# Kernel optimization log

Measured on AMD Instinct MI355X. Metric: run time of the kernel, lower is better.

Reference implementation:

```python
import jax, jax.numpy as jnp
import numpy as np

COMMITMENT_COST = 0.25

def _conv(x, w, stride, pad):
    return jax.lax.conv_general_dilated(
        x, w, window_strides=(stride, stride),
        padding=((pad, pad), (pad, pad)),
        dimension_numbers=("NCHW", "OIHW", "NCHW"))

def _gelu(x):
    return jax.nn.gelu(x, approximate=False)

def setup_inputs() -> dict:
    key = jax.random.key(0)
    ks = jax.random.split(key, 9)
    def w(k, shape):
        fan_in = shape[1] * shape[2] * shape[3]
        return jax.random.normal(k, shape, jnp.float32) / jnp.sqrt(fan_in)
    return {
        "x": jax.random.normal(ks[0], (32, 3, 256, 256), jnp.float32),
        "enc_w1": w(ks[1], (64, 3, 5, 5)),
        "enc_w2": w(ks[2], (64, 64, 5, 5)),
        "enc_w3": w(ks[3], (64, 64, 2, 2)),
        "dec_w1": w(ks[4], (512, 64, 2, 2)),
        "dec_w2": w(ks[5], (256, 512, 2, 2)),
        "dec_w3": w(ks[6], (256, 256, 2, 2)),
        "codes": jax.random.normal(ks[7], (24, 64), jnp.float32),
        "ema_count": jax.random.uniform(ks[8], (24,), jnp.float32) + 0.1,
    }

def reference(x, enc_w1, enc_w2, enc_w3, dec_w1, dec_w2, dec_w3, codes, ema_count):
    # ---- encoder: 256 -> 128 -> 64 -> 63, channels 3 -> 64 ----
    z = _conv(x, enc_w1, 2, 2)
    z = _gelu(z)
    z = _conv(z, enc_w2, 2, 2)
    z = _gelu(z)
    z = _conv(z, enc_w3, 1, 0)          # [B, 64, 63, 63]

    # ---- VQ codebook (EMA variant: commitment loss only) ----
    B, C, H, W = z.shape
    zf = jnp.transpose(z, (0, 2, 3, 1)).reshape(-1, C)          # [N, C]
    # squared L2 distances to each code
    d = (jnp.sum(zf * zf, axis=1, keepdims=True)
         - 2.0 * zf @ codes.T
         + jnp.sum(codes * codes, axis=1))                       # [N, K]
    idx = jnp.argmin(d, axis=1)                                  # [N]
    zq = codes[idx].reshape(B, H, W, C).transpose(0, 3, 1, 2)    # [B, C, H, W]

    vq_loss = COMMITMENT_COST * jnp.mean(
        (jax.lax.stop_gradient(zq) - z) ** 2)
    # straight-through estimator
    z_hat = z + jax.lax.stop_gradient(zq - z)

    # code probabilities from EMA cluster counts, gathered per position
    probs = ema_count / jnp.sum(ema_count)                       # [K]
    z_probs = probs[idx].reshape(B, H, W)                        # [B, H, W]

    # ---- decoder: 63 -> 64 -> 63 -> 64, channels 64 -> 512 -> 256 -> 256 ----
    y = _conv(z_hat, dec_w1, 1, 1)
    y = _gelu(y)
    y = _conv(y, dec_w2, 1, 0)
    y = _gelu(y)
    x_hat = _conv(y, dec_w3, 1, 1)      # [B, 256, 64, 64]

    return (x_hat, z_probs, vq_loss)
```

## Files before the change

### kernel.cpp

```cpp
#include <hip/hip_runtime.h>
#include <hip/hip_bf16.h>


#define DEV_INLINE __device__ __forceinline__

typedef __attribute__((ext_vector_type(8))) short bf16x8;
typedef __attribute__((ext_vector_type(4))) float f32x4;

#define GLL16(g, l) __builtin_amdgcn_global_load_lds(                      \
    (const __attribute__((address_space(1))) void*)(g),                    \
    (__attribute__((address_space(3))) void*)(l), 16, 0, 0)

DEV_INLINE float gelu_exact(float v) {
    return 0.5f * v * (1.0f + erff(v * 0.70710678118654752440f));
}

__global__ void wtf_k(const float* __restrict__ w, float* __restrict__ wt,
                      int C, int total) {
    int t = blockIdx.x * 256 + threadIdx.x;
    if (t >= total) return;
    int oc = t & 63;
    int rest = t >> 6;
    int tap = rest % 25, c = rest / 25;
    wt[t] = w[(oc * C + c) * 25 + tap];
}

template<int C, int IH, int IW>
__global__ __launch_bounds__(256) void conv5s2_t(
    const float* __restrict__ xg,
    const float* __restrict__ wt,
    float* __restrict__ outg) {
    constexpr int OH = IH / 2, OW = IW / 2;
    __shared__ float xin[35 * 36];
    __shared__ float wl[1600];
    const int tid = threadIdx.x;
    const int n = blockIdx.z;
    const int OY0 = blockIdx.y * 16, OX0 = blockIdx.x * 16;
    const int IY0 = OY0 * 2 - 2, IX0 = OX0 * 2 - 2;
    const int og = tid & 3;
    const int pg = tid >> 2;
    const int py = (pg >> 3) * 2, px = (pg & 7) * 2;
    const int ry = py * 2, rx = px * 2;

    f32x4 a00 = {0,0,0,0}, a01 = a00, a02 = a00, a03 = a00;
    f32x4 a10 = a00, a11 = a00, a12 = a00, a13 = a00;
    f32x4 a20 = a00, a21 = a00, a22 = a00, a23 = a00;
    f32x4 a30 = a00, a31 = a00, a32 = a00, a33 = a00;

    const float* xn = xg + (size_t)n * C * IH * IW;
    for (int c = 0; c < C; ++c) {
        {
            const float4* wsrc = (const float4*)(wt + c * 1600);
            float4* wdst = (float4*)wl;
            wdst[tid] = wsrc[tid];
            if (tid < 144) wdst[256 + tid] = wsrc[256 + tid];
        }
        const float* zc = xn + (size_t)c * IH * IW;
        for (int i = tid; i < 1225; i += 256) {
            int r = i / 35, cl = i - r * 35;
            int iy = IY0 + r, ix = IX0 + cl;
            float v = 0.f;
            if ((unsigned)iy < (unsigned)IH && (unsigned)ix < (unsigned)IW)
                v = zc[(size_t)iy * IW + ix];
            xin[r * 36 + cl] = v;
        }
        __syncthreads();
#pragma unroll
        for (int ky = 0; ky < 5; ++ky) {
            const float* r0 = xin + (ry + ky) * 36 + rx;
            const float* r1 = r0 + 72;
#pragma unroll
            for (int kx = 0; kx < 5; ++kx) {
                const f32x4* wq = (const f32x4*)(wl + (ky * 5 + kx) * 64 + og * 16);
                f32x4 w0 = wq[0], w1 = wq[1], w2 = wq[2], w3 = wq[3];
                float xA = r0[kx], xB = r0[kx + 2];
                float xC = r1[kx], xD = r1[kx + 2];
                a00 += xA * w0; a01 += xA * w1; a02 += xA * w2; a03 += xA * w3;
                a10 += xB * w0; a11 += xB * w1; a12 += xB * w2; a13 += xB * w3;
                a20 += xC * w0; a21 += xC * w1; a22 += xC * w2; a23 += xC * w3;
                a30 += xD * w0; a31 += xD * w1; a32 += xD * w2; a33 += xD * w3;
            }
        }
        __syncthreads();
    }
    const int ocb = og * 16;
#define CSTORE(v, oy, ox, q) {                                                \
        float* o = outg + (((size_t)n * 64 + ocb + (q) * 4) * OH + (oy)) * OW \
                   + (ox);                                                    \
        o[0]               = gelu_exact((v).x);                               \
        o[(size_t)OH * OW]     = gelu_exact((v).y);                           \
        o[(size_t)2 * OH * OW] = gelu_exact((v).z);                           \
        o[(size_t)3 * OH * OW] = gelu_exact((v).w); }
    CSTORE(a00, OY0 + py,     OX0 + px,     0); CSTORE(a01, OY0 + py,     OX0 + px,     1);
    CSTORE(a02, OY0 + py,     OX0 + px,     2); CSTORE(a03, OY0 + py,     OX0 + px,     3);
    CSTORE(a10, OY0 + py,     OX0 + px + 1, 0); CSTORE(a11, OY0 + py,     OX0 + px + 1, 1);
    CSTORE(a12, OY0 + py,     OX0 + px + 1, 2); CSTORE(a13, OY0 + py,     OX0 + px + 1, 3);
    CSTORE(a20, OY0 + py + 1, OX0 + px,     0); CSTORE(a21, OY0 + py + 1, OX0 + px,     1);
    CSTORE(a22, OY0 + py + 1, OX0 + px,     2); CSTORE(a23, OY0 + py + 1, OX0 + px,     3);
    CSTORE(a30, OY0 + py + 1, OX0 + px + 1, 0); CSTORE(a31, OY0 + py + 1, OX0 + px + 1, 1);
    CSTORE(a32, OY0 + py + 1, OX0 + px + 1, 2); CSTORE(a33, OY0 + py + 1, OX0 + px + 1, 3);
#undef CSTORE
}

template<int C, int IH, int IW>
__global__ __launch_bounds__(256, 4) void conv5s2_g(
    const float* __restrict__ xg,
    const float* __restrict__ wt,
    float* __restrict__ outg) {
    constexpr int OH = IH / 2, OW = IW / 2;
    __shared__ float xp[760];
    const int tid = threadIdx.x;
    const int n = blockIdx.z;
    const int OY0 = blockIdx.y * 8, OX0 = blockIdx.x * 16;
    const int IY0 = OY0 * 2 - 2, IX0 = OX0 * 2 - 2;
    const int og = tid & 15;
    const int pg = tid >> 4;
    const int py = (pg >> 2) * 2;
    const int px = (pg & 3) * 4;
    const int ry = py * 2;

    int  sG[3]; int sL[3]; bool sIn[3]; bool sWr[3];
#pragma unroll
    for (int k = 0; k < 3; ++k) {
        int s = tid + k * 256;
        int r = s / 36, cl = s - r * 36;
        int iy = IY0 + r, ix = IX0 + cl;
        sWr[k] = (s < 684);
        sIn[k] = sWr[k] && ((unsigned)iy < (unsigned)IH) &&
                 ((unsigned)ix < (unsigned)IW);
        sG[k] = sIn[k] ? (iy * IW + ix) : 0;
        sL[k] = sWr[k] ? ((cl & 1) * 380 + r * 20 + (cl >> 1)) : 0;
    }

    const float* xn = xg + (size_t)n * C * IH * IW;
    const float* wtb = wt + og * 4;

    f32x4 a00 = {0,0,0,0}, a01 = a00, a02 = a00, a03 = a00;
    f32x4 a10 = a00, a11 = a00, a12 = a00, a13 = a00;

    for (int c = 0; c < C; ++c) {
        const float* zc = xn + (size_t)c * IH * IW;
#pragma unroll
        for (int k = 0; k < 3; ++k) {
            if (sWr[k]) {
                float v = sIn[k] ? zc[sG[k]] : 0.f;
                xp[sL[k]] = v;
            }
        }
        __syncthreads();

        const float* wc = wtb + (size_t)c * 1600;
#define PICK8(Qa, Qb, i) ((i) < 4 ? (Qa)[(i) & 3] : (Qb)[(i) & 3])
#define XV(R, kx, jj) (((kx) & 1)                                           \
        ? PICK8(O##R##0, O##R##1, (jj) + ((kx) >> 1))                       \
        : PICK8(E##R##0, E##R##1, (jj) + ((kx) >> 1)))
#pragma unroll
        for (int ky = 0; ky < 5; ++ky) {
            f32x4 w0 = *(const f32x4*)(wc + (ky * 5 + 0) * 64);
            f32x4 w1 = *(const f32x4*)(wc + (ky * 5 + 1) * 64);
            f32x4 w2 = *(const f32x4*)(wc + (ky * 5 + 2) * 64);
            f32x4 w3 = *(const f32x4*)(wc + (ky * 5 + 3) * 64);
            f32x4 w4 = *(const f32x4*)(wc + (ky * 5 + 4) * 64);
            const float* e0 = xp + (ry + ky) * 20 + px;
            const float* o0 = e0 + 380;
            const float* e1 = e0 + 40;
            const float* o1 = o0 + 40;
            const f32x4 E00 = *(const f32x4*)e0, E01 = *(const f32x4*)(e0 + 4);
            const f32x4 O00 = *(const f32x4*)o0, O01 = *(const f32x4*)(o0 + 4);
            const f32x4 E10 = *(const f32x4*)e1, E11 = *(const f32x4*)(e1 + 4);
            const f32x4 O10 = *(const f32x4*)o1, O11 = *(const f32x4*)(o1 + 4);
#pragma unroll
            for (int kx = 0; kx < 5; ++kx) {
                const f32x4 wv = (kx == 0) ? w0 : (kx == 1) ? w1
                               : (kx == 2) ? w2 : (kx == 3) ? w3 : w4;
                float xA = XV(0, kx, 0), xB = XV(0, kx, 1);
                float xC = XV(0, kx, 2), xD = XV(0, kx, 3);
                float xE = XV(1, kx, 0), xF = XV(1, kx, 1);
                float xG = XV(1, kx, 2), xH = XV(1, kx, 3);
                a00 += xA * wv; a01 += xB * wv; a02 += xC * wv; a03 += xD * wv;
                a10 += xE * wv; a11 += xF * wv; a12 += xG * wv; a13 += xH * wv;
            }
        }
#undef XV
#undef PICK8
        __syncthreads();
    }

    const size_t HW = (size_t)OH * OW;
#pragma unroll
    for (int j = 0; j < 4; ++j) {
        float* o = outg + ((size_t)n * 64 + og * 4 + j) * HW
                   + (size_t)(OY0 + py) * OW + (OX0 + px);
        f32x4 t0, t1;
        t0[0] = gelu_exact(a00[j]); t0[1] = gelu_exact(a01[j]);
        t0[2] = gelu_exact(a02[j]); t0[3] = gelu_exact(a03[j]);
        t1[0] = gelu_exact(a10[j]); t1[1] = gelu_exact(a11[j]);
        t1[2] = gelu_exact(a12[j]); t1[3] = gelu_exact(a13[j]);
        *(f32x4*)o = t0;
        *(f32x4*)(o + OW) = t1;
    }
}

__global__ void conv3_k(const float* __restrict__ z2,
                        const float* __restrict__ w,
                        float* __restrict__ z) {
    __shared__ float wl[1024];
    const int oc0 = blockIdx.y * 4;
    for (int i = threadIdx.x; i < 1024; i += 256) {
        int j = i & 3, r = i >> 2;
        wl[i] = w[(oc0 + j) * 256 + r];
    }
    __syncthreads();
    const int s = blockIdx.x * 256 + threadIdx.x;
    if (s >= 3969) return;
    const int n = blockIdx.z;
    const int oy = s / 63, ox = s % 63;
    const float4* wv = (const float4*)wl;
    float a0 = 0.f, a1 = 0.f, a2 = 0.f, a3 = 0.f;
    const float* zn = z2 + n * 64 * 4096;
    for (int c = 0; c < 64; ++c) {
        const float* zc = zn + c * 4096;
#pragma unroll
        for (int tap = 0; tap < 4; ++tap) {
            int iy = oy + (tap >> 1), ix = ox + (tap & 1);
            float xv = zc[iy * 64 + ix];
            float4 wq = wv[c * 4 + tap];
            a0 += xv * wq.x; a1 += xv * wq.y; a2 += xv * wq.z; a3 += xv * wq.w;
        }
    }
    int obase = (n * 64 + oc0) * 3969 + s;
    z[obase]            = a0;
    z[obase + 3969]     = a1;
    z[obase + 2 * 3969] = a2;
    z[obase + 3 * 3969] = a3;
}

__global__ void vq_k(const float* __restrict__ z,
                     const float* __restrict__ codes,
                     const float* __restrict__ ema,
                     int* __restrict__ idxO,
                     float* __restrict__ zprobsO,
                     float* __restrict__ lossO) {
    __shared__ float cl[1536];
    __shared__ float cn[24];
    __shared__ float pr[24];
    for (int i = threadIdx.x; i < 1536; i += 256) cl[i] = codes[i];
    if (threadIdx.x < 24) pr[threadIdx.x] = ema[threadIdx.x];
    __syncthreads();
    if (threadIdx.x < 24) {
        float sm = 0.f;
        for (int c = 0; c < 64; ++c) { float v = cl[threadIdx.x * 64 + c]; sm += v * v; }
        cn[threadIdx.x] = sm;
    }
    __syncthreads();
    int t = blockIdx.x * 256 + threadIdx.x;
    float l = 0.f;
    if (t < 127008) {
        int b = t / 3969, s = t - b * 3969;
        const float* zp = z + (b * 64) * 3969 + s;
        float zv[64];
        float zn = 0.f;
#pragma unroll
        for (int c = 0; c < 64; ++c) { float v = zp[c * 3969]; zv[c] = v; zn += v * v; }
        float best = 1e30f; int bi = 0;
        for (int k = 0; k < 24; ++k) {
            float dot = 0.f;
#pragma unroll
            for (int c = 0; c < 64; ++c) dot += zv[c] * cl[k * 64 + c];
            float d = zn - 2.f * dot + cn[k];
            if (d < best) { best = d; bi = k; }
        }
        idxO[t] = bi;
        float psum = 0.f;
        for (int k = 0; k < 24; ++k) psum += pr[k];
        zprobsO[t] = pr[bi] / psum;
        for (int c = 0; c < 64; ++c) { float dd = cl[bi * 64 + c] - zv[c]; l += dd * dd; }
    }
    for (int off = 32; off; off >>= 1) l += __shfl_down(l, off, 64);
    if ((threadIdx.x & 63) == 0) atomicAdd(lossO, l);
}

__global__ void dtab_k(const float* __restrict__ codes,
                       const float* __restrict__ w1,
                       float* __restrict__ D) {
    int t = blockIdx.x * 256 + threadIdx.x;
    if (t >= 24 * 4 * 512) return;
    int oc = t & 511, tap = (t >> 9) & 3, k = t >> 11;
    float acc = 0.f;
    for (int c = 0; c < 64; ++c)
        acc += codes[k * 64 + c] * w1[oc * 256 + c * 4 + tap];
    D[t] = acc;
}

__global__ void wt_k(const float* __restrict__ w, __hip_bfloat16* __restrict__ wT,
                     int cl2, int total) {
    int t = blockIdx.x * 256 + threadIdx.x;
    if (t >= total) return;
    int c = t & ((1 << cl2) - 1);
    int tap = (t >> cl2) & 3;
    int oc = t >> (cl2 + 2);
    wT[t] = __float2bfloat16(w[((oc << cl2) + c) * 4 + tap]);
}

__global__ void dec1_k(const int* __restrict__ idx,
                       const float* __restrict__ D,
                       __hip_bfloat16* __restrict__ y1) {
    const int pos = blockIdx.x;
    const int n = pos >> 12, rem = pos & 4095;
    const int iy = rem >> 6, ix = rem & 63;
    const int* idn = idx + n * 3969;
    const int t = threadIdx.x;
    float ax = 0.f, ay = 0.f;
#pragma unroll
    for (int tap = 0; tap < 4; ++tap) {
        int py = iy - 1 + (tap >> 1), px = ix - 1 + (tap & 1);
        if ((unsigned)py < 63u && (unsigned)px < 63u) {
            int k = idn[py * 63 + px];
            float2 v = ((const float2*)(D + (k * 4 + tap) * 512))[t];
            ax += v.x; ay += v.y;
        }
    }
    __hip_bfloat162 o;
    o.x = __float2bfloat16(gelu_exact(ax));
    o.y = __float2bfloat16(gelu_exact(ay));
    ((__hip_bfloat162*)(y1 + (size_t)pos * 512))[t] = o;
}

__global__ __launch_bounds__(256) void dec2_mfma(
    const __hip_bfloat16* __restrict__ y1,
    const __hip_bfloat16* __restrict__ wT,
    const __hip_bfloat16* __restrict__ zp,
    __hip_bfloat16* __restrict__ y2)
{
    __shared__ __hip_bfloat16 As[128 * 32];
    __shared__ __hip_bfloat16 Bs[128 * 32];
    const int tid = threadIdx.x;
    const int wave = tid >> 6, lane = tid & 63;
    const int quad = lane >> 4, l15 = lane & 15;
    const int m0 = blockIdx.x * 128;
    const int oc0 = blockIdx.y * 128;
    const int sub = tid & 3;

    const char* pA[2];
    const char* pB[2];
#pragma unroll
    for (int j = 0; j < 2; ++j) {
        int slot = j * 64 + (tid >> 2);
        int pp = m0 + slot;
        if (pp < 127008) {
            int n = pp / 3969; int r = pp - n * 3969;
            int oy = r / 63;  int ox = r - oy * 63;
            pA[j] = (const char*)y1 + (size_t)((n * 64 + oy) * 64 + ox) * 1024 + sub * 16;
        } else {
            pA[j] = (const char*)zp;
        }
        pB[j] = (const char*)wT + (size_t)(oc0 + slot) * 4096 + sub * 16;
    }
    char* ldsA[2] = {(char*)As + wave * 1024, (char*)As + 4096 + wave * 1024};
    char* ldsB[2] = {(char*)Bs + wave * 1024, (char*)Bs + 4096 + wave * 1024};

    f32x4 acc[4][4] = {};
    const int wm = (wave & 1) * 64;
    const int wn = (wave >> 1) * 64;

#pragma unroll
    for (int tap = 0; tap < 4; ++tap) {
        const int toff = ((tap >> 1) * 64 + (tap & 1)) * 1024;
        for (int kk = 0; kk < 16; ++kk) {
            const int cb = kk * 64;
            GLL16(pA[0] + toff + cb, ldsA[0]);
            GLL16(pA[1] + toff + cb, ldsA[1]);
            GLL16(pB[0] + tap * 1024 + cb, ldsB[0]);
            GLL16(pB[1] + tap * 1024 + cb, ldsB[1]);
            __syncthreads();
            bf16x8 af[4], bf[4];
#pragma unroll
            for (int mi = 0; mi < 4; ++mi)
                af[mi] = *(const bf16x8*)((const char*)As + (wm + mi * 16 + l15) * 64 + quad * 16);
#pragma unroll
            for (int ni = 0; ni < 4; ++ni)
                bf[ni] = *(const bf16x8*)((const char*)Bs + (wn + ni * 16 + l15) * 64 + quad * 16);
#pragma unroll
            for (int mi = 0; mi < 4; ++mi)
#pragma unroll
                for (int ni = 0; ni < 4; ++ni)
                    acc[mi][ni] = __builtin_amdgcn_mfma_f32_16x16x32_bf16(
                        af[mi], bf[ni], acc[mi][ni], 0, 0, 0);
            __syncthreads();
        }
    }
#pragma unroll
    for (int mi = 0; mi < 4; ++mi)
#pragma unroll
        for (int r = 0; r < 4; ++r) {
            int pos = m0 + wm + mi * 16 + quad * 4 + r;
            if (pos < 127008) {
#pragma unroll
                for (int ni = 0; ni < 4; ++ni) {
                    int oc = oc0 + wn + ni * 16 + l15;
                    y2[(size_t)pos * 256 + oc] =
                        __float2bfloat16(gelu_exact(acc[mi][ni][r]));
                }
            }
        }
}

__global__ __launch_bounds__(256) void dec3_mfma(
    const __hip_bfloat16* __restrict__ y2,
    const __hip_bfloat16* __restrict__ wT,
    const __hip_bfloat16* __restrict__ zp,
    float* __restrict__ out)
{
    __shared__ __hip_bfloat16 As[128 * 32];
    __shared__ __hip_bfloat16 Bs[128 * 32];
    const int tid = threadIdx.x;
    const int wave = tid >> 6, lane = tid & 63;
    const int quad = lane >> 4, l15 = lane & 15;
    const int p0 = blockIdx.x * 128;
    const int oc0 = blockIdx.y * 128;
    const int sub = tid & 3;

    const char* pW[2];
    const char* pP[4][2];
#pragma unroll
    for (int j = 0; j < 2; ++j) {
        int slot = j * 64 + (tid >> 2);
        pW[j] = (const char*)wT + (size_t)(oc0 + slot) * 2048 + sub * 16;
        int pp = p0 + slot;
        int n = pp >> 12, rem = pp & 4095;
        int OY = rem >> 6, OX = rem & 63;
#pragma unroll
        for (int tap = 0; tap < 4; ++tap) {
            int iy = OY - 1 + (tap >> 1), ix = OX - 1 + (tap & 1);
            if ((unsigned)iy < 63u && (unsigned)ix < 63u)
                pP[tap][j] = (const char*)y2 + (size_t)(n * 3969 + iy * 63 + ix) * 512 + sub * 16;
            else
                pP[tap][j] = (const char*)zp;
        }
    }
    char* ldsA[2] = {(char*)As + wave * 1024, (char*)As + 4096 + wave * 1024};
    char* ldsB[2] = {(char*)Bs + wave * 1024, (char*)Bs + 4096 + wave * 1024};

    f32x4 acc[4][4] = {};
    const int wm = (wave & 1) * 64;
    const int wn = (wave >> 1) * 64;

#pragma unroll
    for (int tap = 0; tap < 4; ++tap) {
        for (int kk = 0; kk < 8; ++kk) {
            const int cb = kk * 64;
            GLL16(pW[0] + tap * 512 + cb, ldsA[0]);
            GLL16(pW[1] + tap * 512 + cb, ldsA[1]);
            GLL16(pP[tap][0] + cb, ldsB[0]);
            GLL16(pP[tap][1] + cb, ldsB[1]);
            __syncthreads();
            bf16x8 af[4], bf[4];
#pragma unroll
            for (int mi = 0; mi < 4; ++mi)
                af[mi] = *(const bf16x8*)((const char*)As + (wm + mi * 16 + l15) * 64 + quad * 16);
#pragma unroll
            for (int ni = 0; ni < 4; ++ni)
                bf[ni] = *(const bf16x8*)((const char*)Bs + (wn + ni * 16 + l15) * 64 + quad * 16);
#pragma unroll
            for (int mi = 0; mi < 4; ++mi)
#pragma unroll
                for (int ni = 0; ni < 4; ++ni)
                    acc[mi][ni] = __builtin_amdgcn_mfma_f32_16x16x32_bf16(
                        af[mi], bf[ni], acc[mi][ni], 0, 0, 0);
            __syncthreads();
        }
    }
    const int n = p0 >> 12;
    const int posLocal0 = (p0 & 4095) + wn;
#pragma unroll
    for (int mi = 0; mi < 4; ++mi)
#pragma unroll
        for (int r = 0; r < 4; ++r) {
            int oc = oc0 + wm + mi * 16 + quad * 4 + r;
            float* orow = out + ((size_t)(n * 256 + oc) << 12);
#pragma unroll
            for (int ni = 0; ni < 4; ++ni)
                orow[posLocal0 + ni * 16 + l15] = acc[mi][ni][r];
        }
}

__global__ void loss_k(const float* __restrict__ lossO, float* __restrict__ out) {
    out[0] = 0.25f * lossO[0] / 8128512.0f;
}

extern "C" void kernel_launch(void* const* d_in, const int* in_sizes, int n_in,
                              void* d_out, int out_size, void* d_ws, size_t ws_size,
                              hipStream_t stream) {
    const float* x     = (const float*)d_in[0];
    const float* ew1   = (const float*)d_in[1];
    const float* ew2   = (const float*)d_in[2];
    const float* ew3   = (const float*)d_in[3];
    const float* dw1   = (const float*)d_in[4];
    const float* dw2   = (const float*)d_in[5];
    const float* dw3   = (const float*)d_in[6];
    const float* codes = (const float*)d_in[7];
    const float* ema   = (const float*)d_in[8];
    float* out = (float*)d_out;

    char* ws = (char*)d_ws;
    float* z1   = (float*)(ws + 0);
    float* z2   = (float*)(ws + 134217728);
    float* z    = (float*)(ws + 167772160);
    int*   idx  = (int*)  (ws + 200286208);
    float* loss = (float*)(ws + 200794240);
    __hip_bfloat16* zp  = (__hip_bfloat16*)(ws + 200794496);
    float* D    = (float*)(ws + 200864128);
    __hip_bfloat16* wT2 = (__hip_bfloat16*)(ws + 201650560);
    __hip_bfloat16* wT3 = (__hip_bfloat16*)(ws + 202699136);
    float* wt2f = (float*)(ws + 201650560);
    float* wt1f = (float*)(ws + 202699136);
    __hip_bfloat16* y1  = (__hip_bfloat16*)(ws + 0);
    __hip_bfloat16* y2  = (__hip_bfloat16*)(ws + 134217728);

    hipMemsetAsync(loss, 0, 4, stream);
    hipMemsetAsync(zp, 0, 69632, stream);

    wtf_k<<<dim3(19), 256, 0, stream>>>(ew1, wt1f, 3, 4800);
    wtf_k<<<dim3(400), 256, 0, stream>>>(ew2, wt2f, 64, 102400);
    conv5s2_t<3, 256, 256><<<dim3(8, 8, 32), 256, 0, stream>>>(x, wt1f, z1);
    conv5s2_g<64, 128, 128><<<dim3(4, 8, 32), 256, 0, stream>>>(z1, wt2f, z2);
    conv3_k<<<dim3(16, 16, 32), 256, 0, stream>>>(z2, ew3, z);
    vq_k<<<dim3(497), 256, 0, stream>>>(z, codes, ema, idx, out + 33554432, loss);
    dtab_k<<<dim3(192), 256, 0, stream>>>(codes, dw1, D);
    wt_k<<<dim3(2048), 256, 0, stream>>>(dw2, wT2, 9, 524288);
    wt_k<<<dim3(1024), 256, 0, stream>>>(dw3, wT3, 8, 262144);
    dec1_k<<<dim3(131072), 256, 0, stream>>>(idx, D, y1);
    dec2_mfma<<<dim3(993, 2), 256, 0, stream>>>(y1, wT2, zp, y2);
    dec3_mfma<<<dim3(1024, 2), 256, 0, stream>>>(y2, wT3, zp, out);
    loss_k<<<1, 1, 0, stream>>>(loss, out + 33681440);
}
```

Before: 1.198 ms.

## Retile 2x2 encoder conv to stage input rows in LDS with register tiling

Replaces the per-pixel 2x2 conv kernel, which re-read the full z2 input once per group of 4 output channels, with a kernel where each block handles one output row of one image. The block stages two input rows for all 64 channels in shared memory, and each thread computes 4 output pixels by 4 channels from pre-transposed weights. This cuts redundant global reads of the input 16-fold, at the cost of an extra weight-transpose kernel and scattered, non-coalesced output stores.

New measurement: 1.161 ms. 1.03x faster.

```diff
diff --git a/kernel.cpp b/kernel.cpp
--- a/kernel.cpp
+++ b/kernel.cpp
@@ -23,6 +23,13 @@
     int rest = t >> 6;
     int tap = rest % 25, c = rest / 25;
     wt[t] = w[(oc * C + c) * 25 + tap];
+}
+
+__global__ void wtf3_k(const float* __restrict__ w, float* __restrict__ wt3) {
+    int t = blockIdx.x * 256 + threadIdx.x;
+    if (t >= 16384) return;
+    int oc = t & 63, tap = (t >> 6) & 3, c = t >> 8;
+    wt3[t] = w[(oc * 64 + c) * 4 + tap];
 }
 
 template<int C, int IH, int IW>
@@ -201,38 +208,61 @@
     }
 }
 
-__global__ void conv3_k(const float* __restrict__ z2,
-                        const float* __restrict__ w,
-                        float* __restrict__ z) {
-    __shared__ float wl[1024];
-    const int oc0 = blockIdx.y * 4;
-    for (int i = threadIdx.x; i < 1024; i += 256) {
-        int j = i & 3, r = i >> 2;
-        wl[i] = w[(oc0 + j) * 256 + r];
+__global__ __launch_bounds__(256) void conv3_t(
+    const float* __restrict__ z2,
+    const float* __restrict__ wt3,
+    float* __restrict__ z) {
+    __shared__ float xs[64 * 144];
+    const int tid = threadIdx.x;
+    const int oy = blockIdx.x;
+    const int n  = blockIdx.y;
+
+    {
+        const float* zn = z2 + (size_t)n * 64 * 4096 + oy * 64;
+#pragma unroll
+        for (int k = 0; k < 8; ++k) {
+            int fid = tid + k * 256;
+            int c = fid >> 5, rem = fid & 31;
+            int r = rem >> 4, q = rem & 15;
+            f32x4 v = *(const f32x4*)(zn + c * 4096 + r * 64 + q * 4);
+            *(f32x4*)(xs + c * 144 + r * 72 + q * 4) = v;
+        }
     }
     __syncthreads();
-    const int s = blockIdx.x * 256 + threadIdx.x;
-    if (s >= 3969) return;
-    const int n = blockIdx.z;
-    const int oy = s / 63, ox = s % 63;
-    const float4* wv = (const float4*)wl;
-    float a0 = 0.f, a1 = 0.f, a2 = 0.f, a3 = 0.f;
-    const float* zn = z2 + n * 64 * 4096;
+
+    const int og  = tid >> 4;
+    const int ox4 = (tid & 15) * 4;
+    f32x4 a0 = {0,0,0,0}, a1 = a0, a2 = a0, a3 = a0;
+    const float* wb = wt3 + og * 4;
+
     for (int c = 0; c < 64; ++c) {
-        const float* zc = zn + c * 4096;
-#pragma unroll
-        for (int tap = 0; tap < 4; ++tap) {
-            int iy = oy + (tap >> 1), ix = ox + (tap & 1);
-            float xv = zc[iy * 64 + ix];
-            float4 wq = wv[c * 4 + tap];
-            a0 += xv * wq.x; a1 += xv * wq.y; a2 += xv * wq.z; a3 += xv * wq.w;
-        }
-    }
-    int obase = (n * 64 + oc0) * 3969 + s;
-    z[obase]            = a0;
-    z[obase + 3969]     = a1;
-    z[obase + 2 * 3969] = a2;
-    z[obase + 3 * 3969] = a3;
+        const float* xc = xs + c * 144 + ox4;
+        const f32x4 X00 = *(const f32x4*)(xc);
+        const f32x4 X01 = *(const f32x4*)(xc + 4);
+        const f32x4 X10 = *(const f32x4*)(xc + 72);
+        const f32x4 X11 = *(const f32x4*)(xc + 76);
+        const float* wc = wb + c * 256;
+        const f32x4 w0 = *(const f32x4*)(wc);
+        const f32x4 w1 = *(const f32x4*)(wc + 64);
+        const f32x4 w2 = *(const f32x4*)(wc + 128);
+        const f32x4 w3 = *(const f32x4*)(wc + 192);
+        a0 += X00[0] * w0; a0 += X00[1] * w1; a0 += X10[0] * w2; a0 += X10[1] * w3;
+        a1 += X00[1] * w0; a1 += X00[2] * w1; a1 += X10[1] * w2; a1 += X10[2] * w3;
+        a2 += X00[2] * w0; a2 += X00[3] * w1; a2 += X10[2] * w2; a2 += X10[3] * w3;
+        a3 += X00[3] * w0; a3 += X01[0] * w1; a3 += X10[3] * w2; a3 += X11[0] * w3;
+    }
+
+#pragma unroll
+    for (int j = 0; j < 4; ++j) {
+        int ox = ox4 + j;
+        if (ox < 63) {
+            const f32x4 aj = (j == 0) ? a0 : (j == 1) ? a1 : (j == 2) ? a2 : a3;
+#pragma unroll
+            for (int i = 0; i < 4; ++i) {
+                z[(((size_t)n * 64 + og * 4 + i) * 63 + oy) * 63 + ox] = aj[i];
+            }
+        }
+    }
 }
 
 __global__ void vq_k(const float* __restrict__ z,
@@ -512,6 +542,7 @@
     float* D    = (float*)(ws + 200864128);
     __hip_bfloat16* wT2 = (__hip_bfloat16*)(ws + 201650560);
     __hip_bfloat16* wT3 = (__hip_bfloat16*)(ws + 202699136);
+    float* wt3f = (float*)(ws + 203223424);
     float* wt2f = (float*)(ws + 201650560);
     float* wt1f = (float*)(ws + 202699136);
     __hip_bfloat16* y1  = (__hip_bfloat16*)(ws + 0);
@@ -522,9 +553,10 @@
 
     wtf_k<<<dim3(19), 256, 0, stream>>>(ew1, wt1f, 3, 4800);
     wtf_k<<<dim3(400), 256, 0, stream>>>(ew2, wt2f, 64, 102400);
+    wtf3_k<<<dim3(64), 256, 0, stream>>>(ew3, wt3f);
     conv5s2_t<3, 256, 256><<<dim3(8, 8, 32), 256, 0, stream>>>(x, wt1f, z1);
     conv5s2_g<64, 128, 128><<<dim3(4, 8, 32), 256, 0, stream>>>(z1, wt2f, z2);
-    conv3_k<<<dim3(16, 16, 32), 256, 0, stream>>>(z2, ew3, z);
+    conv3_t<<<dim3(63, 32), 256, 0, stream>>>(z2, wt3f, z);
     vq_k<<<dim3(497), 256, 0, stream>>>(z, codes, ema, idx, out + 33554432, loss);
     dtab_k<<<dim3(192), 256, 0, stream>>>(codes, dw1, D);
     wt_k<<<dim3(2048), 256, 0, stream>>>(dw2, wT2, 9, 524288);
```
